# Optimization experiments

Hardware: AMD Instinct MI355X
Metric: run time of the kernel (lower is better)

Reference implementation:

```python
import jax, jax.numpy as jnp
import numpy as np

N = 20000
E = 640000
R = 8          # num_rels == num_bases (basis regularizer with num_bases=-1)
B = 8
IN_SIZE = 128
HID = 256      # 4 * fea_dimen
FEA = 64
TIME = 2880
POI = 12


def setup_inputs() -> dict:
    key = jax.random.key(0)
    ks = jax.random.split(key, 20)
    s = 0.02
    inp = {
        'src': jax.random.randint(ks[0], (E,), 0, N),
        'dst': jax.random.randint(ks[1], (E,), 0, N),
        'etype': jax.random.randint(ks[2], (E,), 0, R),
        'poi_distribution': jax.random.normal(ks[3], (N, POI), jnp.float32),
        'time_distribution': jax.random.normal(ks[4], (N, TIME), jnp.float32),
        'road_feature': jax.random.normal(ks[5], (N, IN_SIZE), jnp.float32),
        # input projections
        'poi_w': jax.random.normal(ks[6], (POI, FEA), jnp.float32) * s,
        'poi_b': jnp.zeros((FEA,), jnp.float32),
        'time_w': jax.random.normal(ks[7], (TIME, 2 * FEA), jnp.float32) * s,
        'time_b': jnp.zeros((2 * FEA,), jnp.float32),
        'road_w': jax.random.normal(ks[8], (IN_SIZE, FEA), jnp.float32) * s,
        'road_b': jnp.zeros((FEA,), jnp.float32),
        # RelGraphConv layer 1 (basis decomposition)
        'basis1': jax.random.normal(ks[9], (B, HID, HID), jnp.float32) * s,
        'coef1': jax.random.normal(ks[10], (R, B), jnp.float32) * s,
        'loop_w1': jax.random.normal(ks[11], (HID, HID), jnp.float32) * s,
        'bias1': jnp.zeros((HID,), jnp.float32),
        # RelGraphConv layer 2
        'basis2': jax.random.normal(ks[12], (B, HID, HID), jnp.float32) * s,
        'coef2': jax.random.normal(ks[13], (R, B), jnp.float32) * s,
        'loop_w2': jax.random.normal(ks[14], (HID, HID), jnp.float32) * s,
        'bias2': jnp.zeros((HID,), jnp.float32),
    }
    return inp


def _rel_graph_conv(h, src, dst, etype, basis, coef, loop_w, bias):
    # W_r = sum_b coef[r,b] * basis[b]  -> (R, HID, HID), small
    W = jnp.einsum('rb,bio->rio', coef, basis)
    # transform every node by every relation weight, then gather per edge
    y = jnp.einsum('ni,rio->nro', h, W)          # (N, R, HID)
    msgs = y[src, etype]                          # (E, HID) gather
    agg = jax.ops.segment_sum(msgs, dst, num_segments=h.shape[0])  # scatter-sum
    return agg + h @ loop_w + bias


def reference(src, dst, etype, poi_distribution, time_distribution, road_feature,
              poi_w, poi_b, time_w, time_b, road_w, road_b,
              basis1, coef1, loop_w1, bias1, basis2, coef2, loop_w2, bias2):
    poi_feat = poi_distribution @ poi_w + poi_b       # (N, 64)
    time_feat = time_distribution @ time_w + time_b   # (N, 128)
    road_feat = road_feature @ road_w + road_b        # (N, 64)
    feat = jnp.concatenate([poi_feat, time_feat, road_feat], axis=1)  # (N, 256)
    h = _rel_graph_conv(feat, src, dst, etype, basis1, coef1, loop_w1, bias1)
    h = jax.nn.relu(h)  # dropout=0.0 -> identity
    h = _rel_graph_conv(h, src, dst, etype, basis2, coef2, loop_w2, bias2)
    return h
```

## Files before the change

kernel.cpp:

```cpp
#include <hip/hip_runtime.h>

#define NN 20000
#define NE 640000
#define NR 8
#define NB 8
#define HID 256
#define KPOI 12
#define KTIME 2880
#define KROAD 128
#define NK (NN * NR)
#define SPLITK 5
#define KCH (KTIME / SPLITK)

typedef __attribute__((ext_vector_type(8))) short bf8_t;
typedef __attribute__((ext_vector_type(4))) float f4_t;

__device__ inline unsigned short f2bf(float f) {
  unsigned int u = __float_as_uint(f);
  u += 0x7FFF + ((u >> 16) & 1);
  return (unsigned short)(u >> 16);
}
__device__ inline float bf2f(unsigned short h) {
  return __uint_as_float((unsigned int)h << 16);
}

__global__ __launch_bounds__(256) void make_WT(const float* __restrict__ coef,
                                               const float* __restrict__ basis,
                                               unsigned short* __restrict__ WT) {
  int idx = blockIdx.x * 256 + threadIdx.x;
  if (idx >= NR * HID * HID) return;
  int r = idx >> 16;
  int o = (idx >> 8) & 255;
  int i = idx & 255;
  float acc = 0.f;
#pragma unroll
  for (int b = 0; b < NB; ++b)
    acc += coef[r * NB + b] * basis[b * HID * HID + i * HID + o];
  WT[idx] = f2bf(acc);
}

__global__ __launch_bounds__(256) void transp_bf16(const float* __restrict__ in,
                                                   unsigned short* __restrict__ out,
                                                   int R, int Cc) {
  int idx = blockIdx.x * 256 + threadIdx.x;
  if (idx >= R * Cc) return;
  int r = idx / Cc, c = idx - r * Cc;
  out[(size_t)c * R + r] = f2bf(in[idx]);
}

#define BK 16
template<int BM, int BN, int TM, int TN>
__global__ __launch_bounds__(256) void sgemm_bf(
    int M, int Nn, int K,
    const float* __restrict__ A, int lda,
    const float* __restrict__ B, int ldb,
    const float* __restrict__ bias,
    unsigned short* __restrict__ C, int ldc)
{
  constexpr int SA = BM + 4;
  constexpr int SB = BN + 4;
  __shared__ float As[BK * SA];
  __shared__ float Bs[BK * SB];
  const int tid = threadIdx.x;
  const int brow = blockIdx.x * BM;
  const int bcol = blockIdx.y * BN;
  constexpr int TCOLS = BN / TN;
  const int row0 = (tid / TCOLS) * TM;
  const int col0 = (tid % TCOLS) * TN;

  float acc[TM][TN] = {};

  for (int kb = 0; kb < K; kb += BK) {
    constexpr int AIT = (BM * 4) / 256;
#pragma unroll
    for (int it = 0; it < AIT; ++it) {
      int i = tid + it * 256;
      int r = i >> 2, q = (i & 3) * 4;
      int grow = brow + r, gk = kb + q;
      if (grow < M && gk + 3 < K) {
        float4 v = *(const float4*)(A + (size_t)grow * lda + gk);
        As[(q + 0) * SA + r] = v.x;
        As[(q + 1) * SA + r] = v.y;
        As[(q + 2) * SA + r] = v.z;
        As[(q + 3) * SA + r] = v.w;
      } else {
#pragma unroll
        for (int j = 0; j < 4; ++j)
          As[(q + j) * SA + r] =
              (grow < M && gk + j < K) ? A[(size_t)grow * lda + gk + j] : 0.f;
      }
    }
    constexpr int BIT = (BN * 4) / 256;
#pragma unroll
    for (int it = 0; it < BIT; ++it) {
      int i = tid + it * 256;
      int k = i / (BN / 4), cq = (i % (BN / 4)) * 4;
      int gk = kb + k, gc = bcol + cq;
      float4 v = {0.f, 0.f, 0.f, 0.f};
      if (gk < K) {
        if (gc + 3 < Nn) {
          v = *(const float4*)(B + (size_t)gk * ldb + gc);
        } else {
#pragma unroll
          for (int j = 0; j < 4; ++j)
            if (gc + j < Nn) (&v.x)[j] = B[(size_t)gk * ldb + gc + j];
        }
      }
      *(float4*)(&Bs[k * SB + cq]) = v;
    }
    __syncthreads();
#pragma unroll
    for (int kk = 0; kk < BK; ++kk) {
      float a[TM], b[TN];
#pragma unroll
      for (int i = 0; i < TM; i += 4)
        *(float4*)(&a[i]) = *(const float4*)(&As[kk * SA + row0 + i]);
#pragma unroll
      for (int j = 0; j < TN; j += 4)
        *(float4*)(&b[j]) = *(const float4*)(&Bs[kk * SB + col0 + j]);
#pragma unroll
      for (int i = 0; i < TM; ++i)
#pragma unroll
        for (int j = 0; j < TN; ++j)
          acc[i][j] += a[i] * b[j];
    }
    __syncthreads();
  }

  float bcache[TN];
#pragma unroll
  for (int j = 0; j < TN; ++j)
    bcache[j] = bias ? bias[bcol + col0 + j] : 0.f;
#pragma unroll
  for (int i = 0; i < TM; ++i) {
    int row = brow + row0 + i;
    if (row >= M) continue;
#pragma unroll
    for (int j = 0; j < TN; ++j) {
      int col = bcol + col0 + j;
      if (col < Nn)
        C[(size_t)row * ldc + col] = f2bf(acc[i][j] + bcache[j]);
    }
  }
}

__global__ __launch_bounds__(256) void mfma_time_sk(
    const float* __restrict__ A,
    const unsigned short* __restrict__ BT,
    float* __restrict__ TP)
{
  __shared__ __align__(16) char ldsA[32 * 128];
  __shared__ __align__(16) char ldsB[128 * 128];
  const int tid = threadIdx.x;
  const int lane = tid & 63;
  const int w = tid >> 6;
  const int brow = blockIdx.x * 32;
  const int kb0 = blockIdx.y * KCH;

  f4_t acc[2][2];
#pragma unroll
  for (int i = 0; i < 2; ++i)
#pragma unroll
    for (int j = 0; j < 2; ++j) acc[i][j] = (f4_t){0.f, 0.f, 0.f, 0.f};

  for (int kb = kb0; kb < kb0 + KCH; kb += 64) {
    {
      int r = tid >> 3, c8 = tid & 7;
      const float* ap = A + (size_t)(brow + r) * KTIME + kb + c8 * 8;
      f4_t v0 = *(const f4_t*)ap;
      f4_t v1 = *(const f4_t*)(ap + 4);
      unsigned short hh[8];
#pragma unroll
      for (int j = 0; j < 4; ++j) { hh[j] = f2bf(v0[j]); hh[4 + j] = f2bf(v1[j]); }
      *(bf8_t*)(ldsA + r * 128 + ((c8 * 16) ^ ((r & 7) << 4))) = *(bf8_t*)hh;
    }
#pragma unroll
    for (int it = 0; it < 4; ++it) {
      int slot = tid + it * 256;
      int r = slot >> 3, c8 = slot & 7;
      bf8_t v = *(const bf8_t*)(BT + (size_t)r * KTIME + kb + c8 * 8);
      *(bf8_t*)(ldsB + r * 128 + ((c8 * 16) ^ ((r & 7) << 4))) = v;
    }
    __syncthreads();
#pragma unroll
    for (int ks = 0; ks < 2; ++ks) {
      const int kbyte = ks * 64 + (lane >> 4) * 16;
      bf8_t af[2], bfr[2];
#pragma unroll
      for (int mi = 0; mi < 2; ++mi) {
        int m = mi * 16 + (lane & 15);
        af[mi] = *(const bf8_t*)(ldsA + m * 128 + (kbyte ^ ((m & 7) << 4)));
      }
#pragma unroll
      for (int ni = 0; ni < 2; ++ni) {
        int n = w * 32 + ni * 16 + (lane & 15);
        bfr[ni] = *(const bf8_t*)(ldsB + n * 128 + (kbyte ^ ((n & 7) << 4)));
      }
#pragma unroll
      for (int mi = 0; mi < 2; ++mi)
#pragma unroll
        for (int ni = 0; ni < 2; ++ni)
          acc[mi][ni] = __builtin_amdgcn_mfma_f32_16x16x32_bf16(
              af[mi], bfr[ni], acc[mi][ni], 0, 0, 0);
    }
    __syncthreads();
  }

  float* tp = TP + (size_t)blockIdx.y * NN * 128;
  const int rq = (lane >> 4) * 4;
  const int cl = lane & 15;
#pragma unroll
  for (int ni = 0; ni < 2; ++ni) {
    int c = w * 32 + ni * 16 + cl;
#pragma unroll
    for (int mi = 0; mi < 2; ++mi) {
#pragma unroll
      for (int j = 0; j < 4; ++j) {
        int row = brow + mi * 16 + rq + j;
        tp[(size_t)row * 128 + c] = acc[mi][ni][j];
      }
    }
  }
}

__global__ __launch_bounds__(256) void time_finish(
    const float* __restrict__ TP, const float* __restrict__ bias,
    unsigned short* __restrict__ featb) {
  int i = blockIdx.x * 256 + threadIdx.x;
  if (i >= NN * 32) return;
  int row = i >> 5, c4 = (i & 31) * 4;
  f4_t s = *(const f4_t*)(TP + (size_t)row * 128 + c4);
#pragma unroll
  for (int k = 1; k < SPLITK; ++k) {
    f4_t v = *(const f4_t*)(TP + (size_t)k * NN * 128 + (size_t)row * 128 + c4);
    s.x += v.x; s.y += v.y; s.z += v.z; s.w += v.w;
  }
  f4_t b = *(const f4_t*)(bias + c4);
  unsigned short h[4] = {f2bf(s.x + b.x), f2bf(s.y + b.y),
                         f2bf(s.z + b.z), f2bf(s.w + b.w)};
  *(ushort4*)(featb + (size_t)row * 256 + 64 + c4) = *(ushort4*)h;
}

__global__ __launch_bounds__(256) void agg_k(
    const int* __restrict__ offs, const unsigned short* __restrict__ ssrc,
    const unsigned short* __restrict__ hin, unsigned short* __restrict__ Z) {
  int w = (blockIdx.x * 256 + threadIdx.x) >> 6;
  int lane = threadIdx.x & 63;
  if (w >= NR * NN) return;
  int q = w / NN;
  int d = w - q * NN;
  int lo = offs[d * NR + q];
  int hi = offs[d * NR + q + 1];
  f4_t az = {0.f, 0.f, 0.f, 0.f};
  int e = lo;
  for (; e + 4 <= hi; e += 4) {
    int s0 = ssrc[e], s1 = ssrc[e + 1], s2 = ssrc[e + 2], s3 = ssrc[e + 3];
    ushort4 u0 = *(const ushort4*)(hin + (size_t)s0 * HID + lane * 4);
    ushort4 u1 = *(const ushort4*)(hin + (size_t)s1 * HID + lane * 4);
    ushort4 u2 = *(const ushort4*)(hin + (size_t)s2 * HID + lane * 4);
    ushort4 u3 = *(const ushort4*)(hin + (size_t)s3 * HID + lane * 4);
    az.x += (bf2f(u0.x) + bf2f(u1.x)) + (bf2f(u2.x) + bf2f(u3.x));
    az.y += (bf2f(u0.y) + bf2f(u1.y)) + (bf2f(u2.y) + bf2f(u3.y));
    az.z += (bf2f(u0.z) + bf2f(u1.z)) + (bf2f(u2.z) + bf2f(u3.z));
    az.w += (bf2f(u0.w) + bf2f(u1.w)) + (bf2f(u2.w) + bf2f(u3.w));
  }
  for (; e < hi; ++e) {
    int s = ssrc[e];
    ushort4 u = *(const ushort4*)(hin + (size_t)s * HID + lane * 4);
    az.x += bf2f(u.x); az.y += bf2f(u.y);
    az.z += bf2f(u.z); az.w += bf2f(u.w);
  }
  unsigned short hz[4] = {f2bf(az.x), f2bf(az.y), f2bf(az.z), f2bf(az.w)};
  *(ushort4*)(Z + (size_t)w * HID + lane * 4) = *(ushort4*)hz;
}

template<int EPI>
__global__ __launch_bounds__(512) void gemm_acc(
    const unsigned short* __restrict__ hbufA,
    const unsigned short* __restrict__ Z,
    const unsigned short* __restrict__ WT,
    const unsigned short* __restrict__ LWT,
    const float* __restrict__ bias,
    float* __restrict__ C, unsigned short* __restrict__ hb)
{
  __shared__ __align__(16) char At[64 * 512];
  __shared__ __align__(16) char Bt[128 * 128];
  const int tid = threadIdx.x;
  const int lane = tid & 63;
  const int w = tid >> 6;
  const int wr = w >> 1;
  const int wc = w & 1;
  const int brow = blockIdx.x * 64;
  const int bcol = blockIdx.y * 128;

  f4_t acc[4];
#pragma unroll
  for (int i = 0; i < 4; ++i) acc[i] = (f4_t){0.f, 0.f, 0.f, 0.f};

#pragma unroll 1
  for (int s = 0; s < NR + 1; ++s) {
    const unsigned short* Asrc = (s == 0) ? hbufA : Z + (size_t)(s - 1) * NN * HID;
    const unsigned short* Wsrc = (s == 0) ? LWT : WT + (size_t)(s - 1) * HID * HID;
#pragma unroll
    for (int it = 0; it < 4; ++it) {
      int slot = tid + it * 512;
      int r = slot >> 5, c16 = slot & 31;
      bf8_t v = {0, 0, 0, 0, 0, 0, 0, 0};
      int grow = brow + r;
      if (grow < NN) v = *(const bf8_t*)(Asrc + (size_t)grow * HID + c16 * 8);
      *(bf8_t*)(At + r * 512 + ((c16 * 16) ^ ((r & 7) << 4))) = v;
    }
    __syncthreads();
#pragma unroll 1
    for (int kc = 0; kc < 4; ++kc) {
#pragma unroll
      for (int it = 0; it < 2; ++it) {
        int slot = tid + it * 512;
        int n = slot >> 3, c8 = slot & 7;
        bf8_t v = *(const bf8_t*)(Wsrc + (size_t)(bcol + n) * HID + kc * 64 + c8 * 8);
        *(bf8_t*)(Bt + n * 128 + ((c8 * 16) ^ ((n & 7) << 4))) = v;
      }
      __syncthreads();
#pragma unroll
      for (int ks = 0; ks < 2; ++ks) {
        const int kbyte = ks * 64 + (lane >> 4) * 16;
        int m = wr * 16 + (lane & 15);
        bf8_t af = *(const bf8_t*)(
            At + m * 512 + ((kc * 128 + kbyte) ^ ((m & 7) << 4)));
#pragma unroll
        for (int ni = 0; ni < 4; ++ni) {
          int n = wc * 64 + ni * 16 + (lane & 15);
          bf8_t bfr = *(const bf8_t*)(Bt + n * 128 + (kbyte ^ ((n & 7) << 4)));
          acc[ni] = __builtin_amdgcn_mfma_f32_16x16x32_bf16(af, bfr, acc[ni], 0, 0, 0);
        }
      }
      __syncthreads();
    }
  }

  const int rq = (lane >> 4) * 4;
  const int cl = lane & 15;
#pragma unroll
  for (int ni = 0; ni < 4; ++ni) {
    int c = bcol + wc * 64 + ni * 16 + cl;
    float bv = bias[c];
#pragma unroll
    for (int j = 0; j < 4; ++j) {
      int row = brow + wr * 16 + rq + j;
      if (row < NN) {
        size_t o = (size_t)row * 256 + c;
        float v = acc[ni][j] + bv;
        if (EPI == 0) C[o] = v;
        else          hb[o] = f2bf(fmaxf(v, 0.f));
      }
    }
  }
}

__global__ __launch_bounds__(256) void hist_k(const int* __restrict__ dst,
                                              const int* __restrict__ et,
                                              int* __restrict__ counts) {
  int e = blockIdx.x * 256 + threadIdx.x;
  if (e < NE) atomicAdd(&counts[dst[e] * NR + et[e]], 1);
}

__global__ __launch_bounds__(256) void scan_block(const int* __restrict__ counts,
                                                  int* __restrict__ offs,
                                                  int* __restrict__ bsums) {
  __shared__ int sh[256];
  int base = blockIdx.x * 1024;
  int t = threadIdx.x;
  int v[4];
  int s = 0;
#pragma unroll
  for (int j = 0; j < 4; ++j) {
    int idx = base + t * 4 + j;
    v[j] = (idx < NK) ? counts[idx] : 0;
    s += v[j];
  }
  sh[t] = s;
  __syncthreads();
  for (int off = 1; off < 256; off <<= 1) {
    int x = (t >= off) ? sh[t - off] : 0;
    __syncthreads();
    sh[t] += x;
    __syncthreads();
  }
  int run = sh[t] - s;
#pragma unroll
  for (int j = 0; j < 4; ++j) {
    int idx = base + t * 4 + j;
    if (idx < NK) offs[idx] = run;
    run += v[j];
  }
  if (t == 255) bsums[blockIdx.x] = sh[255];
}

__global__ __launch_bounds__(256) void scan_bsums(int* __restrict__ bsums, int nblk) {
  __shared__ int sh[256];
  int t = threadIdx.x;
  int own = (t < nblk) ? bsums[t] : 0;
  sh[t] = own;
  __syncthreads();
  for (int off = 1; off < 256; off <<= 1) {
    int x = (t >= off) ? sh[t - off] : 0;
    __syncthreads();
    sh[t] += x;
    __syncthreads();
  }
  int ex = sh[t] - own;
  if (t < nblk) bsums[t] = ex;
}

__global__ __launch_bounds__(256) void add_base(int* __restrict__ offs,
                                                const int* __restrict__ bsums) {
  int idx = blockIdx.x * 256 + threadIdx.x;
  if (idx < NK) offs[idx] += bsums[idx >> 10];
  if (idx == NK) offs[NK] = NE;
}

__global__ __launch_bounds__(256) void copy_int(const int* __restrict__ a,
                                                int* __restrict__ b, int n) {
  int i = blockIdx.x * 256 + threadIdx.x;
  if (i < n) b[i] = a[i];
}

__global__ __launch_bounds__(256) void fill_k(const int* __restrict__ src,
                                              const int* __restrict__ dst,
                                              const int* __restrict__ et,
                                              int* __restrict__ cursor,
                                              unsigned short* __restrict__ ssrc) {
  int e = blockIdx.x * 256 + threadIdx.x;
  if (e < NE) {
    int key = dst[e] * NR + et[e];
    int p = atomicAdd(&cursor[key], 1);
    ssrc[p] = (unsigned short)src[e];
  }
}

extern "C" void kernel_launch(void* const* d_in, const int* in_sizes, int n_in,
                              void* d_out, int out_size, void* d_ws, size_t ws_size,
                              hipStream_t stream) {
  const int*   srcp      = (const int*)d_in[0];
  const int*   dstp      = (const int*)d_in[1];
  const int*   etypep    = (const int*)d_in[2];
  const float* poi_dist  = (const float*)d_in[3];
  const float* time_dist = (const float*)d_in[4];
  const float* road_feat = (const float*)d_in[5];
  const float* poi_w     = (const float*)d_in[6];
  const float* poi_b     = (const float*)d_in[7];
  const float* time_w    = (const float*)d_in[8];
  const float* time_b    = (const float*)d_in[9];
  const float* road_w    = (const float*)d_in[10];
  const float* road_b    = (const float*)d_in[11];
  const float* basis1    = (const float*)d_in[12];
  const float* coef1     = (const float*)d_in[13];
  const float* loop_w1   = (const float*)d_in[14];
  const float* bias1     = (const float*)d_in[15];
  const float* basis2    = (const float*)d_in[16];
  const float* coef2     = (const float*)d_in[17];
  const float* loop_w2   = (const float*)d_in[18];
  const float* bias2     = (const float*)d_in[19];

  float* out = (float*)d_out;

  char* ws = (char*)d_ws;
  unsigned short* WT     = (unsigned short*)(ws);
  unsigned short* LWT1   = (unsigned short*)(ws + 1048576);
  unsigned short* LWT2   = (unsigned short*)(ws + 1179648);
  unsigned short* TWT    = (unsigned short*)(ws + 1310720);
  unsigned short* hbuf   = (unsigned short*)(ws + 2048000);
  unsigned short* Z      = (unsigned short*)(ws + 12288000);
  float*          TP     = (float*)(ws + 94208000);
  int*            offs   = (int*)  (ws + 145408000);
  int*            bsums  = (int*)  (ws + 146048016);
  unsigned short* ssrc   = (unsigned short*)(ws + 146049040);
  int*            counts = (int*)Z;
  int*            cursor = (int*)TP;

  dim3 blk(256);
  const int MG64 = (NN + 63) / 64;

  hipMemsetAsync(counts, 0, NK * sizeof(int), stream);
  hist_k<<<NE / 256, blk, 0, stream>>>(dstp, etypep, counts);
  scan_block<<<(NK + 1023) / 1024, blk, 0, stream>>>(counts, offs, bsums);
  scan_bsums<<<1, blk, 0, stream>>>(bsums, (NK + 1023) / 1024);
  add_base<<<(NK + 1 + 255) / 256, blk, 0, stream>>>(offs, bsums);
  copy_int<<<(NK + 255) / 256, blk, 0, stream>>>(offs, cursor, NK);
  fill_k<<<NE / 256, blk, 0, stream>>>(srcp, dstp, etypep, cursor, ssrc);

  transp_bf16<<<(HID * HID + 255) / 256, blk, 0, stream>>>(loop_w1, LWT1, HID, HID);
  transp_bf16<<<(HID * HID + 255) / 256, blk, 0, stream>>>(loop_w2, LWT2, HID, HID);
  transp_bf16<<<(KTIME * 128 + 255) / 256, blk, 0, stream>>>(time_w, TWT, KTIME, 128);
  make_WT<<<(NR * HID * HID + 255) / 256, blk, 0, stream>>>(coef1, basis1, WT);

  sgemm_bf<64, 64, 4, 4><<<dim3(MG64, 1), blk, 0, stream>>>(
      NN, 64, KPOI, poi_dist, KPOI, poi_w, 64, poi_b, hbuf + 0, HID);
  mfma_time_sk<<<dim3(NN / 32, SPLITK), blk, 0, stream>>>(time_dist, TWT, TP);
  time_finish<<<(NN * 32 + 255) / 256, blk, 0, stream>>>(TP, time_b, hbuf);
  sgemm_bf<64, 64, 4, 4><<<dim3(MG64, 1), blk, 0, stream>>>(
      NN, 64, KROAD, road_feat, KROAD, road_w, 64, road_b, hbuf + 192, HID);

  agg_k<<<(NR * NN) / 4, blk, 0, stream>>>(offs, ssrc, hbuf, Z);
  gemm_acc<2><<<dim3(MG64, 2), 512, 0, stream>>>(hbuf, Z, WT, LWT1, bias1,
                                                 nullptr, hbuf);

  make_WT<<<(NR * HID * HID + 255) / 256, blk, 0, stream>>>(coef2, basis2, WT);
  agg_k<<<(NR * NN) / 4, blk, 0, stream>>>(offs, ssrc, hbuf, Z);
  gemm_acc<0><<<dim3(MG64, 2), 512, 0, stream>>>(hbuf, Z, WT, LWT2, bias2,
                                                 out, nullptr);
}
```

Before: 459.8 us.

## Use full-width 32-row GEMM tiles and merge small setup kernels

The relational accumulation GEMM now gives each block 32 rows and all 256 output columns, instead of 64 rows by 128 columns. Each large Z/h row panel is therefore read from memory once rather than twice, at the cost of staging the whole weight slice per block. This layout also means a block only overwrites the hbuf rows it has already read, removing a cross-block read/write hazard in the in-place layer-1 epilogue. Both layers' relation weights and both loop-weight transposes are built in single launches, and the cursor copy is folded into the scan's add-base kernel, cutting launch count.

```diff
diff --git a/kernel.cpp b/kernel.cpp
--- a/kernel.cpp
+++ b/kernel.cpp
@@ -24,19 +24,34 @@
   return __uint_as_float((unsigned int)h << 16);
 }
 
-__global__ __launch_bounds__(256) void make_WT(const float* __restrict__ coef,
-                                               const float* __restrict__ basis,
-                                               unsigned short* __restrict__ WT) {
+__global__ __launch_bounds__(256) void make_WT12(
+    const float* __restrict__ coef1, const float* __restrict__ basis1,
+    const float* __restrict__ coef2, const float* __restrict__ basis2,
+    unsigned short* __restrict__ WT) {
   int idx = blockIdx.x * 256 + threadIdx.x;
-  if (idx >= NR * HID * HID) return;
   int r = idx >> 16;
   int o = (idx >> 8) & 255;
   int i = idx & 255;
+  const float* coef  = (r < NR) ? coef1 : coef2;
+  const float* basis = (r < NR) ? basis1 : basis2;
+  int rr = r & 7;
   float acc = 0.f;
 #pragma unroll
   for (int b = 0; b < NB; ++b)
-    acc += coef[r * NB + b] * basis[b * HID * HID + i * HID + o];
+    acc += coef[rr * NB + b] * basis[b * HID * HID + i * HID + o];
   WT[idx] = f2bf(acc);
+}
+
+__global__ __launch_bounds__(256) void transp_LW(
+    const float* __restrict__ w1, const float* __restrict__ w2,
+    unsigned short* __restrict__ L1, unsigned short* __restrict__ L2) {
+  int idx = blockIdx.x * 256 + threadIdx.x;
+  int sel = idx >> 16;
+  int j = idx & 65535;
+  int r = j >> 8, c = j & 255;
+  const float* in = sel ? w2 : w1;
+  unsigned short* out = sel ? L2 : L1;
+  out[c * HID + r] = f2bf(in[j]);
 }
 
 __global__ __launch_bounds__(256) void transp_bf16(const float* __restrict__ in,
@@ -283,15 +298,14 @@
     const float* __restrict__ bias,
     float* __restrict__ C, unsigned short* __restrict__ hb)
 {
-  __shared__ __align__(16) char At[64 * 512];
-  __shared__ __align__(16) char Bt[128 * 128];
+  __shared__ __align__(16) char At[32 * 512];
+  __shared__ __align__(16) char Bt[256 * 128];
   const int tid = threadIdx.x;
   const int lane = tid & 63;
   const int w = tid >> 6;
-  const int wr = w >> 1;
-  const int wc = w & 1;
-  const int brow = blockIdx.x * 64;
-  const int bcol = blockIdx.y * 128;
+  const int wr = w >> 2;
+  const int wc = w & 3;
+  const int brow = blockIdx.x * 32;
 
   f4_t acc[4];
 #pragma unroll
@@ -302,22 +316,20 @@
     const unsigned short* Asrc = (s == 0) ? hbufA : Z + (size_t)(s - 1) * NN * HID;
     const unsigned short* Wsrc = (s == 0) ? LWT : WT + (size_t)(s - 1) * HID * HID;
 #pragma unroll
-    for (int it = 0; it < 4; ++it) {
+    for (int it = 0; it < 2; ++it) {
       int slot = tid + it * 512;
       int r = slot >> 5, c16 = slot & 31;
-      bf8_t v = {0, 0, 0, 0, 0, 0, 0, 0};
-      int grow = brow + r;
-      if (grow < NN) v = *(const bf8_t*)(Asrc + (size_t)grow * HID + c16 * 8);
+      bf8_t v = *(const bf8_t*)(Asrc + (size_t)(brow + r) * HID + c16 * 8);
       *(bf8_t*)(At + r * 512 + ((c16 * 16) ^ ((r & 7) << 4))) = v;
     }
     __syncthreads();
 #pragma unroll 1
     for (int kc = 0; kc < 4; ++kc) {
 #pragma unroll
-      for (int it = 0; it < 2; ++it) {
+      for (int it = 0; it < 4; ++it) {
         int slot = tid + it * 512;
         int n = slot >> 3, c8 = slot & 7;
-        bf8_t v = *(const bf8_t*)(Wsrc + (size_t)(bcol + n) * HID + kc * 64 + c8 * 8);
+        bf8_t v = *(const bf8_t*)(Wsrc + (size_t)n * HID + kc * 64 + c8 * 8);
         *(bf8_t*)(Bt + n * 128 + ((c8 * 16) ^ ((n & 7) << 4))) = v;
       }
       __syncthreads();
@@ -342,17 +354,15 @@
   const int cl = lane & 15;
 #pragma unroll
   for (int ni = 0; ni < 4; ++ni) {
-    int c = bcol + wc * 64 + ni * 16 + cl;
+    int c = wc * 64 + ni * 16 + cl;
     float bv = bias[c];
 #pragma unroll
     for (int j = 0; j < 4; ++j) {
       int row = brow + wr * 16 + rq + j;
-      if (row < NN) {
-        size_t o = (size_t)row * 256 + c;
-        float v = acc[ni][j] + bv;
-        if (EPI == 0) C[o] = v;
-        else          hb[o] = f2bf(fmaxf(v, 0.f));
-      }
+      size_t o = (size_t)row * 256 + c;
+      float v = acc[ni][j] + bv;
+      if (EPI == 0) C[o] = v;
+      else          hb[o] = f2bf(fmaxf(v, 0.f));
     }
   }
 }
@@ -413,16 +423,15 @@
 }
 
 __global__ __launch_bounds__(256) void add_base(int* __restrict__ offs,
-                                                const int* __restrict__ bsums) {
+                                                const int* __restrict__ bsums,
+                                                int* __restrict__ cursor) {
   int idx = blockIdx.x * 256 + threadIdx.x;
-  if (idx < NK) offs[idx] += bsums[idx >> 10];
+  if (idx < NK) {
+    int v = offs[idx] + bsums[idx >> 10];
+    offs[idx] = v;
+    cursor[idx] = v;
+  }
   if (idx == NK) offs[NK] = NE;
-}
-
-__global__ __launch_bounds__(256) void copy_int(const int* __restrict__ a,
-                                                int* __restrict__ b, int n) {
-  int i = blockIdx.x * 256 + threadIdx.x;
-  if (i < n) b[i] = a[i];
 }
 
 __global__ __launch_bounds__(256) void fill_k(const int* __restrict__ src,
@@ -465,16 +474,17 @@
   float* out = (float*)d_out;
 
   char* ws = (char*)d_ws;
-  unsigned short* WT     = (unsigned short*)(ws);
-  unsigned short* LWT1   = (unsigned short*)(ws + 1048576);
-  unsigned short* LWT2   = (unsigned short*)(ws + 1179648);
-  unsigned short* TWT    = (unsigned short*)(ws + 1310720);
-  unsigned short* hbuf   = (unsigned short*)(ws + 2048000);
-  unsigned short* Z      = (unsigned short*)(ws + 12288000);
-  float*          TP     = (float*)(ws + 94208000);
-  int*            offs   = (int*)  (ws + 145408000);
-  int*            bsums  = (int*)  (ws + 146048016);
-  unsigned short* ssrc   = (unsigned short*)(ws + 146049040);
+  unsigned short* WT1    = (unsigned short*)(ws);
+  unsigned short* WT2    = (unsigned short*)(ws + 1048576);
+  unsigned short* LWT1   = (unsigned short*)(ws + 2097152);
+  unsigned short* LWT2   = (unsigned short*)(ws + 2228224);
+  unsigned short* TWT    = (unsigned short*)(ws + 2359296);
+  unsigned short* hbuf   = (unsigned short*)(ws + 3096576);
+  unsigned short* Z      = (unsigned short*)(ws + 13336576);
+  float*          TP     = (float*)(ws + 95256576);
+  int*            offs   = (int*)  (ws + 146456576);
+  int*            bsums  = (int*)  (ws + 147096592);
+  unsigned short* ssrc   = (unsigned short*)(ws + 147097616);
   int*            counts = (int*)Z;
   int*            cursor = (int*)TP;
 
@@ -485,14 +495,13 @@
   hist_k<<<NE / 256, blk, 0, stream>>>(dstp, etypep, counts);
   scan_block<<<(NK + 1023) / 1024, blk, 0, stream>>>(counts, offs, bsums);
   scan_bsums<<<1, blk, 0, stream>>>(bsums, (NK + 1023) / 1024);
-  add_base<<<(NK + 1 + 255) / 256, blk, 0, stream>>>(offs, bsums);
-  copy_int<<<(NK + 255) / 256, blk, 0, stream>>>(offs, cursor, NK);
+  add_base<<<(NK + 1 + 255) / 256, blk, 0, stream>>>(offs, bsums, cursor);
   fill_k<<<NE / 256, blk, 0, stream>>>(srcp, dstp, etypep, cursor, ssrc);
 
-  transp_bf16<<<(HID * HID + 255) / 256, blk, 0, stream>>>(loop_w1, LWT1, HID, HID);
-  transp_bf16<<<(HID * HID + 255) / 256, blk, 0, stream>>>(loop_w2, LWT2, HID, HID);
+  transp_LW<<<2 * HID * HID / 256, blk, 0, stream>>>(loop_w1, loop_w2, LWT1, LWT2);
   transp_bf16<<<(KTIME * 128 + 255) / 256, blk, 0, stream>>>(time_w, TWT, KTIME, 128);
-  make_WT<<<(NR * HID * HID + 255) / 256, blk, 0, stream>>>(coef1, basis1, WT);
+  make_WT12<<<2 * NR * HID * HID / 256, blk, 0, stream>>>(coef1, basis1,
+                                                          coef2, basis2, WT1);
 
   sgemm_bf<64, 64, 4, 4><<<dim3(MG64, 1), blk, 0, stream>>>(
       NN, 64, KPOI, poi_dist, KPOI, poi_w, 64, poi_b, hbuf + 0, HID);
@@ -502,11 +511,10 @@
       NN, 64, KROAD, road_feat, KROAD, road_w, 64, road_b, hbuf + 192, HID);
 
   agg_k<<<(NR * NN) / 4, blk, 0, stream>>>(offs, ssrc, hbuf, Z);
-  gemm_acc<2><<<dim3(MG64, 2), 512, 0, stream>>>(hbuf, Z, WT, LWT1, bias1,
-                                                 nullptr, hbuf);
-
-  make_WT<<<(NR * HID * HID + 255) / 256, blk, 0, stream>>>(coef2, basis2, WT);
+  gemm_acc<2><<<NN / 32, 512, 0, stream>>>(hbuf, Z, WT1, LWT1, bias1,
+                                           nullptr, hbuf);
+
   agg_k<<<(NR * NN) / 4, blk, 0, stream>>>(offs, ssrc, hbuf, Z);
-  gemm_acc<0><<<dim3(MG64, 2), 512, 0, stream>>>(hbuf, Z, WT, LWT2, bias2,
-                                                 out, nullptr);
-}
+  gemm_acc<0><<<NN / 32, 512, 0, stream>>>(hbuf, Z, WT2, LWT2, bias2,
+                                           out, nullptr);
+}
```

After: 461.6 us. About the same (+0.4%).
